# Performance work log

Measured on AMD Instinct MI355X. Metric: run time of the kernel, lower is better.

The kernel has to match this reference:

```python
import jax, jax.numpy as jnp
import numpy as np

MIN_LOGITS_VALUE = -2.3819763e+38
MAX_WAVELENGTH = 10000


def _apply_rope(inputs, positions):
    # inputs: [b, t, n, h]; positions: [b, t]. RoPE on first half of h.
    x_rope, x = jnp.split(inputs, 2, axis=-1)
    pos = positions[:, :, None, None].astype(jnp.float32)  # [b, t, 1, 1]
    freq_exponents = 2.0 * jnp.arange(x_rope.shape[-1] // 2) / x_rope.shape[-1]
    inv_freq = 1.0 / (MAX_WAVELENGTH ** freq_exponents)
    sinusoid = pos * inv_freq  # [b, t, 1, h/2]
    sin = jnp.sin(sinusoid).astype(inputs.dtype)
    cos = jnp.cos(sinusoid).astype(inputs.dtype)
    first, second = jnp.split(x_rope, 2, axis=-1)
    return jnp.concatenate(
        [first * cos - second * sin, second * cos + first * sin, x], axis=-1)


def _forward_pass_mask(segment_pos, window_size):
    # segment_pos: [b, t]; 0 marks a segment start.
    segment_ids = jnp.cumsum(segment_pos == 0, axis=-1)  # [b, t]
    t = segment_pos.shape[-1]
    positions = jnp.arange(t)
    same_segment = segment_ids[:, :, None] == segment_ids[:, None, :]
    causal = positions[:, None] >= positions[None, :]
    window = positions[:, None] <= positions[None, :] + window_size
    return same_segment & (causal & window)[None]  # [b, t, t]


def setup_inputs() -> dict:
    key = jax.random.key(0)
    ks = jax.random.split(key, 6)
    B, T, W, N = 2, 2048, 2048, 16
    H = W // N
    x = jax.random.normal(ks[0], (B, T, W), jnp.float32)
    sc = 1.0 / np.sqrt(W).astype(np.float32)
    w_q = jax.random.normal(ks[1], (W, W), jnp.float32) * sc
    w_k = jax.random.normal(ks[2], (W, H), jnp.float32) * sc
    w_v = jax.random.normal(ks[3], (W, H), jnp.float32) * sc
    w_out = jax.random.normal(ks[4], (W, W), jnp.float32) * sc
    b_out = jnp.zeros((W,), jnp.float32)
    segment_pos = jnp.tile(jnp.arange(T, dtype=jnp.int32)[None], (B, 1))
    return {"x": x, "w_q": w_q, "w_k": w_k, "w_v": w_v, "w_out": w_out,
            "b_out": b_out, "segment_pos": segment_pos,
            "num_heads": N, "window_size": 1024}


def reference(x, w_q, w_k, w_v, w_out, b_out, segment_pos, num_heads, window_size):
    b, t, width = x.shape
    head_dim = width // num_heads
    # Projections: MQA -> keys/values are single-head [b, t, head_dim].
    q = (x @ w_q).reshape(b, t, num_heads, head_dim)
    k = (x @ w_k)[:, :, None, :]  # [b, t, 1, h]
    v = x @ w_v                   # [b, t, h]
    q = _apply_rope(q, segment_pos)
    k = _apply_rope(k, segment_pos)[:, :, 0]  # [b, t, h]
    logits = jnp.einsum('btnh,bsh->bnts', q, k) * (head_dim ** -0.5)
    mask = _forward_pass_mask(segment_pos, window_size)  # [b, t, t]
    masked = jnp.where(mask[:, None], logits, MIN_LOGITS_VALUE).astype(jnp.float32)
    probs = jax.nn.softmax(masked, axis=-1).astype(x.dtype)
    encoded = jnp.einsum('bnts,bsh->btnh', probs, v).reshape(b, t, width)
    return encoded @ w_out + b_out
```

## Files before the change

kernel.cpp:

```cpp
#include <hip/hip_runtime.h>
#include <hip/hip_bf16.h>
#include <stdint.h>

typedef __attribute__((ext_vector_type(8))) short short8;
typedef __attribute__((ext_vector_type(4))) float f32x4;

__device__ __forceinline__ float bf2f(short u) {
  return __uint_as_float(((unsigned)(unsigned short)u) << 16);
}
__device__ __forceinline__ short f2bf(float f) {
  unsigned x = __float_as_uint(f);
  unsigned r = (x + 0x7fffu + ((x >> 16) & 1u)) >> 16;
  return (short)r;
}

__device__ __forceinline__ void gload_lds16(const short* g, short* l) {
  __builtin_amdgcn_global_load_lds(
      (const __attribute__((address_space(1))) void*)g,
      (__attribute__((address_space(3))) void*)l, 16, 0, 0);
}

__global__ void cast_x_bf16(const float* __restrict__ in, short* __restrict__ out, int n8) {
  int i = blockIdx.x * blockDim.x + threadIdx.x;
  if (i >= n8) return;
  const float4* p = (const float4*)in + (size_t)i * 2;
  float4 a = p[0], b = p[1];
  short8 o;
  o[0] = f2bf(a.x); o[1] = f2bf(a.y); o[2] = f2bf(a.z); o[3] = f2bf(a.w);
  o[4] = f2bf(b.x); o[5] = f2bf(b.y); o[6] = f2bf(b.z); o[7] = f2bf(b.w);
  *((short8*)out + i) = o;
}

__global__ void transpose_cast(const float* __restrict__ in, int R, int C,
                               short* __restrict__ out, int row_off, int ldo) {
  __shared__ float tile[32][33];
  int c0 = blockIdx.x * 32, r0 = blockIdx.y * 32;
  int tx = threadIdx.x, ty = threadIdx.y;
#pragma unroll
  for (int i = 0; i < 4; ++i)
    tile[ty + i * 8][tx] = in[(size_t)(r0 + ty + i * 8) * C + (c0 + tx)];
  __syncthreads();
#pragma unroll
  for (int i = 0; i < 4; ++i)
    out[(size_t)(row_off + c0 + ty + i * 8) * ldo + (r0 + tx)] =
        f2bf(tile[tx][ty + i * 8]);
}

template <int OUT_F32>
__global__ __launch_bounds__(256)
void gemm_bt(const short* __restrict__ A, const short* __restrict__ Bt,
             int M, int N, int K, int ldc,
             short* __restrict__ outb, float* __restrict__ outf,
             const float* __restrict__ bias) {
  __shared__ short As[128 * 64];
  __shared__ short Bs[128 * 64];
  const int tid = threadIdx.x, lane = tid & 63;
  const int wr = tid >> 7, wc = (tid >> 6) & 1;
  const int l15 = lane & 15, l4 = lane >> 4;
  const int m0 = blockIdx.y * 128, n0 = blockIdx.x * 128;
  f32x4 acc[4][4] = {};
  for (int k0 = 0; k0 < K; k0 += 64) {
#pragma unroll
    for (int iss = 0; iss < 4; ++iss) {
      int c = iss * 256 + tid;
      int row = c >> 3, q = c & 7;
      gload_lds16(A + (size_t)(m0 + row) * K + k0 + q * 8,
                  As + iss * 2048 + (tid & 192) * 8);
      gload_lds16(Bt + (size_t)(n0 + row) * K + k0 + q * 8,
                  Bs + iss * 2048 + (tid & 192) * 8);
    }
    __syncthreads();
#pragma unroll
    for (int kk = 0; kk < 2; ++kk) {
      short8 a[4], b[4];
#pragma unroll
      for (int mi = 0; mi < 4; ++mi)
        a[mi] = *(const short8*)(As + (wr * 64 + mi * 16 + l15) * 64 + kk * 32 + l4 * 8);
#pragma unroll
      for (int ni = 0; ni < 4; ++ni)
        b[ni] = *(const short8*)(Bs + (wc * 64 + ni * 16 + l15) * 64 + kk * 32 + l4 * 8);
#pragma unroll
      for (int mi = 0; mi < 4; ++mi)
#pragma unroll
        for (int ni = 0; ni < 4; ++ni)
          acc[mi][ni] = __builtin_amdgcn_mfma_f32_16x16x32_bf16(a[mi], b[ni], acc[mi][ni], 0, 0, 0);
    }
    __syncthreads();
  }
#pragma unroll
  for (int mi = 0; mi < 4; ++mi)
#pragma unroll
    for (int ni = 0; ni < 4; ++ni)
#pragma unroll
      for (int r = 0; r < 4; ++r) {
        int row = m0 + wr * 64 + mi * 16 + l4 * 4 + r;
        int col = n0 + wc * 64 + ni * 16 + l15;
        if (OUT_F32)
          outf[(size_t)row * ldc + col] = acc[mi][ni][r] + bias[col];
        else
          outb[(size_t)row * ldc + col] = f2bf(acc[mi][ni][r]);
      }
}

__global__ void rope_kernel(short* __restrict__ qkv, const int* __restrict__ segpos,
                            int nheads, int hd, int ld) {
  const int row = blockIdx.x;
  const float pos = (float)segpos[row];
  short* base = qkv + (size_t)row * ld;
  const int quarter = hd >> 2;
  const int npairs_q = nheads * quarter;
  const int total = npairs_q + quarter;
  for (int p = threadIdx.x; p < total; p += blockDim.x) {
    int i, off;
    if (p < npairs_q) { off = (p >> 5) * hd; i = p & 31; }
    else              { off = nheads * hd;  i = p - npairs_q; }
    float ang = pos * exp2f(-(float)i * (13.287712379549449f / (float)quarter));
    float s, c;
    sincosf(ang, &s, &c);
    float a = bf2f(base[off + i]);
    float b = bf2f(base[off + quarter + i]);
    base[off + i]           = f2bf(a * c - b * s);
    base[off + quarter + i] = f2bf(b * c + a * s);
  }
}

#define SWZV(h) ((((h) ^ ((h) >> 3)) & 7) << 4)
__global__ __launch_bounds__(512)
void attn_kernel(const short* __restrict__ qkv, short* __restrict__ enc,
                 const int* __restrict__ wsz_p, int T, int nheads, int nqt, int bhc) {
  const int window = wsz_p[0];
  const int i = blockIdx.x;
  const int qt = nqt - 1 - (i / bhc);
  const int bh = i % bhc;
  const int b = bh / nheads, n = bh % nheads;
  const int tid = threadIdx.x, lane = tid & 63, w = tid >> 6;
  const int l15 = lane & 15, l4 = lane >> 4;
  const int q0 = qt * 128;
  const size_t rowbase = (size_t)b * T;
  const int LD = nheads * 128 + 256;
  const int kcol = nheads * 128;
  const float CC = 0.08838834764831845f * 1.4426950408889634f;

  __shared__ short Ks[64 * 128];
  __shared__ short Vt[128 * 64];
  __shared__ short Pl[8][16 * 72];

  short8 qf[4];
  {
    const short* qptr = qkv + (rowbase + q0 + w * 16 + l15) * LD + n * 128 + l4 * 8;
#pragma unroll
    for (int kk = 0; kk < 4; ++kk) qf[kk] = *(const short8*)(qptr + kk * 32);
  }
  f32x4 o[8] = {};
  float mrow[4], lrow[4];
#pragma unroll
  for (int r = 0; r < 4; ++r) { mrow[r] = -1e30f; lrow[r] = 0.f; }

  const int tmin = q0 + w * 16, tmax = tmin + 15;
  int st_lo = q0 - window; if (st_lo < 0) st_lo = 0; st_lo >>= 6;
  const int st_hi = (q0 + 127) >> 6;

  short8 kreg[2], vreg[2];
  auto load_tile = [&](int s0) {
#pragma unroll
    for (int it = 0; it < 2; ++it) {
      int c = it * 512 + tid;
      int r = c >> 4, cg = c & 15;
      const short* rowp = qkv + (rowbase + s0 + r) * (size_t)LD + kcol;
      kreg[it] = *(const short8*)(rowp + cg * 8);
      vreg[it] = *(const short8*)(rowp + 128 + cg * 8);
    }
  };
  auto store_tile = [&]() {
#pragma unroll
    for (int it = 0; it < 2; ++it) {
      int c = it * 512 + tid;
      int r = c >> 4, cg = c & 15;
      *(short8*)((char*)Ks + ((r * 256 + cg * 16) ^ ((r & 7) << 4))) = kreg[it];
      int h0 = cg * 8;
#pragma unroll
      for (int j = 0; j < 8; ++j) {
        int h = h0 + j;
        *(short*)((char*)Vt + ((h * 128 + r * 2) ^ SWZV(h))) = vreg[it][j];
      }
    }
  };

  load_tile(st_lo * 64);
  store_tile();
  __syncthreads();

  for (int st = st_lo; st <= st_hi; ++st) {
    const int s0 = st * 64;
    const bool more = (st < st_hi);
    if (more) load_tile(s0 + 64);

    const bool active = (s0 <= tmax) && (tmin <= s0 + 63 + window);
    if (active) {
      f32x4 sacc[4];
      __builtin_amdgcn_s_setprio(1);
#pragma unroll
      for (int si = 0; si < 4; ++si) {
        f32x4 acc = {};
        int srow = si * 16 + l15;
#pragma unroll
        for (int kk = 0; kk < 4; ++kk) {
          int byt = (srow * 256 + (kk * 32 + l4 * 8) * 2) ^ ((srow & 7) << 4);
          short8 kf = *(const short8*)((const char*)Ks + byt);
          acc = __builtin_amdgcn_mfma_f32_16x16x32_bf16(qf[kk], kf, acc, 0, 0, 0);
        }
        sacc[si] = acc;
      }
      __builtin_amdgcn_s_setprio(0);

      const int trow0 = q0 + w * 16 + l4 * 4;
      float mt[4];
#pragma unroll
      for (int r = 0; r < 4; ++r) mt[r] = -1e30f;
#pragma unroll
      for (int si = 0; si < 4; ++si) {
        int s = s0 + si * 16 + l15;
#pragma unroll
        for (int r = 0; r < 4; ++r) {
          int t = trow0 + r;
          float v = (s <= t && t <= s + window) ? sacc[si][r] : -1e30f;
          sacc[si][r] = v;
          mt[r] = fmaxf(mt[r], v);
        }
      }
#pragma unroll
      for (int r = 0; r < 4; ++r)
#pragma unroll
        for (int off = 1; off < 16; off <<= 1)
          mt[r] = fmaxf(mt[r], __shfl_xor(mt[r], off));

      bool dfr = true;
#pragma unroll
      for (int r = 0; r < 4; ++r) dfr = dfr && ((mt[r] - mrow[r]) * CC <= 8.0f);
      const bool defer = __all(dfr);
      float fac[4];
      if (!defer) {
#pragma unroll
        for (int r = 0; r < 4; ++r) {
          float mnew = fmaxf(mrow[r], mt[r]);
          fac[r] = exp2f((mrow[r] - mnew) * CC);
          mrow[r] = mnew;
        }
      }
      float psum[4];
#pragma unroll
      for (int r = 0; r < 4; ++r) psum[r] = 0.f;
#pragma unroll
      for (int si = 0; si < 4; ++si)
#pragma unroll
        for (int r = 0; r < 4; ++r) {
          float p = exp2f((sacc[si][r] - mrow[r]) * CC);
          psum[r] += p;
          Pl[w][(l4 * 4 + r) * 72 + si * 16 + l15] = f2bf(p);
        }
#pragma unroll
      for (int r = 0; r < 4; ++r) {
#pragma unroll
        for (int off = 1; off < 16; off <<= 1)
          psum[r] += __shfl_xor(psum[r], off);
        if (!defer) lrow[r] = lrow[r] * fac[r] + psum[r];
        else        lrow[r] += psum[r];
      }
      if (!defer) {
#pragma unroll
        for (int nt = 0; nt < 8; ++nt)
#pragma unroll
          for (int r = 0; r < 4; ++r) o[nt][r] *= fac[r];
      }

      __builtin_amdgcn_s_setprio(1);
#pragma unroll
      for (int kk = 0; kk < 2; ++kk) {
        short8 pf = *(const short8*)(&Pl[w][l15 * 72 + kk * 32 + l4 * 8]);
#pragma unroll
        for (int nt = 0; nt < 8; ++nt) {
          int h = nt * 16 + l15;
          int vb = (h * 128 + kk * 64 + l4 * 16) ^ SWZV(h);
          short8 vf = *(const short8*)((const char*)Vt + vb);
          o[nt] = __builtin_amdgcn_mfma_f32_16x16x32_bf16(pf, vf, o[nt], 0, 0, 0);
        }
      }
      __builtin_amdgcn_s_setprio(0);
    }
    __syncthreads();
    if (more) store_tile();
    __syncthreads();
  }

#pragma unroll
  for (int nt = 0; nt < 8; ++nt)
#pragma unroll
    for (int r = 0; r < 4; ++r) {
      size_t row = rowbase + q0 + w * 16 + l4 * 4 + r;
      int col = n * 128 + nt * 16 + l15;
      enc[row * (size_t)(nheads * 128) + col] = f2bf(o[nt][r] / lrow[r]);
    }
}

extern "C" void kernel_launch(void* const* d_in, const int* in_sizes, int n_in,
                              void* d_out, int out_size, void* d_ws, size_t ws_size,
                              hipStream_t stream) {
  const float* x     = (const float*)d_in[0];
  const float* w_q   = (const float*)d_in[1];
  const float* w_k   = (const float*)d_in[2];
  const float* w_v   = (const float*)d_in[3];
  const float* w_out = (const float*)d_in[4];
  const float* b_out = (const float*)d_in[5];
  const int* segpos  = (const int*)d_in[6];
  const int* wsz     = (const int*)d_in[8];
  float* out = (float*)d_out;

  const int BT = in_sizes[6];
  const int W  = in_sizes[5];
  const int H  = in_sizes[2] / W;
  const int NH = W / H;
  const int T  = 2048;
  const int NQKV = W + 2 * H;

  char* ws = (char*)d_ws;
  short* xb    = (short*)ws;
  short* wqkvT = (short*)(ws + (size_t)BT * W * 2);
  short* woutT = (short*)(ws + (size_t)(BT * W + NQKV * W) * 2);
  short* qkv   = (short*)(ws + (size_t)(BT * W + NQKV * W + W * W) * 2);
  short* enc   = xb;

  int n8 = BT * W / 8;
  cast_x_bf16<<<(n8 + 255) / 256, 256, 0, stream>>>(x, xb, n8);

  dim3 tb(32, 8);
  transpose_cast<<<dim3(W / 32, W / 32), tb, 0, stream>>>(w_q, W, W, wqkvT, 0, W);
  transpose_cast<<<dim3(H / 32, W / 32), tb, 0, stream>>>(w_k, W, H, wqkvT, W, W);
  transpose_cast<<<dim3(H / 32, W / 32), tb, 0, stream>>>(w_v, W, H, wqkvT, W + H, W);
  transpose_cast<<<dim3(W / 32, W / 32), tb, 0, stream>>>(w_out, W, W, woutT, 0, W);

  gemm_bt<0><<<dim3(NQKV / 128, BT / 128), 256, 0, stream>>>(
      xb, wqkvT, BT, NQKV, W, NQKV, qkv, nullptr, nullptr);

  rope_kernel<<<BT, 256, 0, stream>>>(qkv, segpos, NH, H, NQKV);

  const int nqt = T / 128;
  const int bhc = (BT / T) * NH;
  attn_kernel<<<nqt * bhc, 512, 0, stream>>>(qkv, enc, wsz, T, NH, nqt, bhc);

  gemm_bt<1><<<dim3(W / 128, BT / 128), 256, 0, stream>>>(
      enc, woutT, BT, W, W, W, nullptr, out, b_out);
}
```

Baseline: 378.7 us.

## Split-K both GEMMs, pre-transpose V, skip mask on fully-visible tiles

Both projection GEMMs now split K in two across a third grid dimension, write fp32 partials and finish with reduction kernels: one fuses the reduce with RoPE and bf16 cast, the other adds the bias. The goal is more blocks to fill the GPU, since each GEMM has only 32x17 or 32x16 tiles. V is transposed once into a [b,h,t] buffer so the attention kernel can store V tiles to LDS with vector writes instead of scalar scatter. Attention also skips per-element masking on tiles that are fully inside the causal window. Costs are extra fp32 partial traffic and extra kernel launches, and the split path only runs when the workspace is large enough.

New measurement: 395.6 us. +4.5%, slower.

```diff
diff --git a/kernel.cpp b/kernel.cpp
--- a/kernel.cpp
+++ b/kernel.cpp
@@ -44,6 +44,20 @@
   for (int i = 0; i < 4; ++i)
     out[(size_t)(row_off + c0 + ty + i * 8) * ldo + (r0 + tx)] =
         f2bf(tile[tx][ty + i * 8]);
+}
+
+__global__ void transpose_v(const short* __restrict__ qkv, short* __restrict__ vT,
+                            int T, int LD, int vcol) {
+  __shared__ short tile[32][33];
+  int t0 = blockIdx.x * 32, h0 = blockIdx.y * 32, b = blockIdx.z;
+  int tx = threadIdx.x, ty = threadIdx.y;
+#pragma unroll
+  for (int i = 0; i < 4; ++i)
+    tile[ty + i * 8][tx] = qkv[((size_t)b * T + t0 + ty + i * 8) * LD + vcol + h0 + tx];
+  __syncthreads();
+#pragma unroll
+  for (int i = 0; i < 4; ++i)
+    vT[((size_t)b * 128 + h0 + ty + i * 8) * T + t0 + tx] = tile[tx][ty + i * 8];
 }
 
 template <int OUT_F32>
@@ -100,6 +114,95 @@
         else
           outb[(size_t)row * ldc + col] = f2bf(acc[mi][ni][r]);
       }
+}
+
+__global__ __launch_bounds__(256)
+void gemm_sk(const short* __restrict__ A, const short* __restrict__ Bt,
+             int M, int N, int K, int ldc, float* __restrict__ pout) {
+  __shared__ short As[128 * 64];
+  __shared__ short Bs[128 * 64];
+  const int tid = threadIdx.x, lane = tid & 63;
+  const int wr = tid >> 7, wc = (tid >> 6) & 1;
+  const int l15 = lane & 15, l4 = lane >> 4;
+  const int m0 = blockIdx.y * 128, n0 = blockIdx.x * 128;
+  const int khalf = K >> 1, kbeg = blockIdx.z * khalf;
+  f32x4 acc[4][4] = {};
+  for (int k0 = kbeg; k0 < kbeg + khalf; k0 += 64) {
+#pragma unroll
+    for (int iss = 0; iss < 4; ++iss) {
+      int c = iss * 256 + tid;
+      int row = c >> 3, q = c & 7;
+      gload_lds16(A + (size_t)(m0 + row) * K + k0 + q * 8,
+                  As + iss * 2048 + (tid & 192) * 8);
+      gload_lds16(Bt + (size_t)(n0 + row) * K + k0 + q * 8,
+                  Bs + iss * 2048 + (tid & 192) * 8);
+    }
+    __syncthreads();
+#pragma unroll
+    for (int kk = 0; kk < 2; ++kk) {
+      short8 a[4], b[4];
+#pragma unroll
+      for (int mi = 0; mi < 4; ++mi)
+        a[mi] = *(const short8*)(As + (wr * 64 + mi * 16 + l15) * 64 + kk * 32 + l4 * 8);
+#pragma unroll
+      for (int ni = 0; ni < 4; ++ni)
+        b[ni] = *(const short8*)(Bs + (wc * 64 + ni * 16 + l15) * 64 + kk * 32 + l4 * 8);
+#pragma unroll
+      for (int mi = 0; mi < 4; ++mi)
+#pragma unroll
+        for (int ni = 0; ni < 4; ++ni)
+          acc[mi][ni] = __builtin_amdgcn_mfma_f32_16x16x32_bf16(a[mi], b[ni], acc[mi][ni], 0, 0, 0);
+    }
+    __syncthreads();
+  }
+  float* po = pout + (size_t)blockIdx.z * M * ldc;
+#pragma unroll
+  for (int mi = 0; mi < 4; ++mi)
+#pragma unroll
+    for (int ni = 0; ni < 4; ++ni)
+#pragma unroll
+      for (int r = 0; r < 4; ++r) {
+        int row = m0 + wr * 64 + mi * 16 + l4 * 4 + r;
+        int col = n0 + wc * 64 + ni * 16 + l15;
+        po[(size_t)row * ldc + col] = acc[mi][ni][r];
+      }
+}
+
+__global__ void reduce_rope(const float* __restrict__ p, short* __restrict__ qkv,
+                            const int* __restrict__ segpos, int rows, int ldc) {
+  const int row = blockIdx.x;
+  const float* r0 = p + (size_t)row * ldc;
+  const float* r1 = p + (size_t)(rows + row) * ldc;
+  short* outr = qkv + (size_t)row * ldc;
+  const float pos = (float)segpos[row];
+  for (int t = threadIdx.x; t < 544; t += 256) {
+    int h = t >> 5, i = t & 31;
+    int off = h * 128;
+    float a = r0[off + i] + r1[off + i];
+    float b = r0[off + 32 + i] + r1[off + 32 + i];
+    float ang = pos * exp2f(-(float)i * (13.287712379549449f / 32.f));
+    float s, c;
+    sincosf(ang, &s, &c);
+    outr[off + i]      = f2bf(a * c - b * s);
+    outr[off + 32 + i] = f2bf(b * c + a * s);
+  }
+  for (int t = threadIdx.x; t < 1216; t += 256) {
+    int col = (t < 1088) ? ((t >> 6) * 128 + 64 + (t & 63)) : (2176 + t - 1088);
+    outr[col] = f2bf(r0[col] + r1[col]);
+  }
+}
+
+__global__ void reduce_bias(const float* __restrict__ p, const float* __restrict__ bias,
+                            float* __restrict__ out, int n, int ldc) {
+  int i = blockIdx.x * 256 + threadIdx.x;
+  if (i * 4 >= n) return;
+  float4 a = ((const float4*)p)[i];
+  float4 b = ((const float4*)(p + n))[i];
+  float4 bb = *(const float4*)(bias + ((i * 4) % ldc));
+  float4 o;
+  o.x = a.x + b.x + bb.x; o.y = a.y + b.y + bb.y;
+  o.z = a.z + b.z + bb.z; o.w = a.w + b.w + bb.w;
+  ((float4*)out)[i] = o;
 }
 
 __global__ void rope_kernel(short* __restrict__ qkv, const int* __restrict__ segpos,
@@ -124,9 +227,9 @@
   }
 }
 
-#define SWZV(h) ((((h) ^ ((h) >> 3)) & 7) << 4)
 __global__ __launch_bounds__(512)
-void attn_kernel(const short* __restrict__ qkv, short* __restrict__ enc,
+void attn_kernel(const short* __restrict__ qkv, const short* __restrict__ vT,
+                 short* __restrict__ enc,
                  const int* __restrict__ wsz_p, int T, int nheads, int nqt, int bhc) {
   const int window = wsz_p[0];
   const int i = blockIdx.x;
@@ -165,24 +268,18 @@
 #pragma unroll
     for (int it = 0; it < 2; ++it) {
       int c = it * 512 + tid;
-      int r = c >> 4, cg = c & 15;
-      const short* rowp = qkv + (rowbase + s0 + r) * (size_t)LD + kcol;
-      kreg[it] = *(const short8*)(rowp + cg * 8);
-      vreg[it] = *(const short8*)(rowp + 128 + cg * 8);
+      kreg[it] = *(const short8*)(qkv + (rowbase + s0 + (c >> 4)) * (size_t)LD + kcol + (c & 15) * 8);
+      vreg[it] = *(const short8*)(vT + ((size_t)b * 128 + (c >> 3)) * T + s0 + (c & 7) * 8);
     }
   };
   auto store_tile = [&]() {
 #pragma unroll
     for (int it = 0; it < 2; ++it) {
       int c = it * 512 + tid;
-      int r = c >> 4, cg = c & 15;
-      *(short8*)((char*)Ks + ((r * 256 + cg * 16) ^ ((r & 7) << 4))) = kreg[it];
-      int h0 = cg * 8;
-#pragma unroll
-      for (int j = 0; j < 8; ++j) {
-        int h = h0 + j;
-        *(short*)((char*)Vt + ((h * 128 + r * 2) ^ SWZV(h))) = vreg[it][j];
-      }
+      int r = c >> 4;
+      *(short8*)((char*)Ks + ((r * 256 + (c & 15) * 16) ^ ((r & 7) << 4))) = kreg[it];
+      int h = c >> 3;
+      *(short8*)((char*)Vt + ((h * 128 + (c & 7) * 16) ^ ((h & 7) << 4))) = vreg[it];
     }
   };
 
@@ -214,18 +311,25 @@
       __builtin_amdgcn_s_setprio(0);
 
       const int trow0 = q0 + w * 16 + l4 * 4;
+      const bool full = (s0 + 63 <= tmin) && (tmax <= s0 + window);
       float mt[4];
-#pragma unroll
-      for (int r = 0; r < 4; ++r) mt[r] = -1e30f;
-#pragma unroll
-      for (int si = 0; si < 4; ++si) {
-        int s = s0 + si * 16 + l15;
-#pragma unroll
-        for (int r = 0; r < 4; ++r) {
-          int t = trow0 + r;
-          float v = (s <= t && t <= s + window) ? sacc[si][r] : -1e30f;
-          sacc[si][r] = v;
-          mt[r] = fmaxf(mt[r], v);
+      if (full) {
+#pragma unroll
+        for (int r = 0; r < 4; ++r)
+          mt[r] = fmaxf(fmaxf(sacc[0][r], sacc[1][r]), fmaxf(sacc[2][r], sacc[3][r]));
+      } else {
+#pragma unroll
+        for (int r = 0; r < 4; ++r) mt[r] = -1e30f;
+#pragma unroll
+        for (int si = 0; si < 4; ++si) {
+          int s = s0 + si * 16 + l15;
+#pragma unroll
+          for (int r = 0; r < 4; ++r) {
+            int t = trow0 + r;
+            float v = (s <= t && t <= s + window) ? sacc[si][r] : -1e30f;
+            sacc[si][r] = v;
+            mt[r] = fmaxf(mt[r], v);
+          }
         }
       }
 #pragma unroll
@@ -280,7 +384,7 @@
 #pragma unroll
         for (int nt = 0; nt < 8; ++nt) {
           int h = nt * 16 + l15;
-          int vb = (h * 128 + kk * 64 + l4 * 16) ^ SWZV(h);
+          int vb = (h * 128 + kk * 64 + l4 * 16) ^ ((h & 7) << 4);
           short8 vf = *(const short8*)((const char*)Vt + vb);
           o[nt] = __builtin_amdgcn_mfma_f32_16x16x32_bf16(pf, vf, o[nt], 0, 0, 0);
         }
@@ -320,14 +424,21 @@
   const int H  = in_sizes[2] / W;
   const int NH = W / H;
   const int T  = 2048;
+  const int B  = BT / T;
   const int NQKV = W + 2 * H;
 
   char* ws = (char*)d_ws;
+  const size_t base =
+      (size_t)(BT * W + NQKV * W + W * W + BT * NQKV) * 2;
   short* xb    = (short*)ws;
   short* wqkvT = (short*)(ws + (size_t)BT * W * 2);
   short* woutT = (short*)(ws + (size_t)(BT * W + NQKV * W) * 2);
   short* qkv   = (short*)(ws + (size_t)(BT * W + NQKV * W + W * W) * 2);
+  short* vTp   = wqkvT;
   short* enc   = xb;
+  float* part  = (float*)(ws + base);
+  const size_t need = base + (size_t)2 * BT * NQKV * 4;
+  const bool split = ws_size >= need;
 
   int n8 = BT * W / 8;
   cast_x_bf16<<<(n8 + 255) / 256, 256, 0, stream>>>(x, xb, n8);
@@ -338,15 +449,29 @@
   transpose_cast<<<dim3(H / 32, W / 32), tb, 0, stream>>>(w_v, W, H, wqkvT, W + H, W);
   transpose_cast<<<dim3(W / 32, W / 32), tb, 0, stream>>>(w_out, W, W, woutT, 0, W);
 
-  gemm_bt<0><<<dim3(NQKV / 128, BT / 128), 256, 0, stream>>>(
-      xb, wqkvT, BT, NQKV, W, NQKV, qkv, nullptr, nullptr);
-
-  rope_kernel<<<BT, 256, 0, stream>>>(qkv, segpos, NH, H, NQKV);
+  if (split) {
+    gemm_sk<<<dim3(NQKV / 128, BT / 128, 2), 256, 0, stream>>>(
+        xb, wqkvT, BT, NQKV, W, NQKV, part);
+    reduce_rope<<<BT, 256, 0, stream>>>(part, qkv, segpos, BT, NQKV);
+  } else {
+    gemm_bt<0><<<dim3(NQKV / 128, BT / 128), 256, 0, stream>>>(
+        xb, wqkvT, BT, NQKV, W, NQKV, qkv, nullptr, nullptr);
+    rope_kernel<<<BT, 256, 0, stream>>>(qkv, segpos, NH, H, NQKV);
+  }
+
+  transpose_v<<<dim3(T / 32, H / 32, B), tb, 0, stream>>>(qkv, vTp, T, NQKV, NH * H + H);
 
   const int nqt = T / 128;
-  const int bhc = (BT / T) * NH;
-  attn_kernel<<<nqt * bhc, 512, 0, stream>>>(qkv, enc, wsz, T, NH, nqt, bhc);
-
-  gemm_bt<1><<<dim3(W / 128, BT / 128), 256, 0, stream>>>(
-      enc, woutT, BT, W, W, W, nullptr, out, b_out);
-}
+  const int bhc = B * NH;
+  attn_kernel<<<nqt * bhc, 512, 0, stream>>>(qkv, vTp, enc, wsz, T, NH, nqt, bhc);
+
+  if (split) {
+    gemm_sk<<<dim3(W / 128, BT / 128, 2), 256, 0, stream>>>(
+        enc, woutT, BT, W, W, W, part);
+    reduce_bias<<<(BT * W / 4 + 255) / 256, 256, 0, stream>>>(
+        part, b_out, out, BT * W, W);
+  } else {
+    gemm_bt<1><<<dim3(W / 128, BT / 128), 256, 0, stream>>>(
+        enc, woutT, BT, W, W, W, nullptr, out, b_out);
+  }
+}
```
